# Kernel tuning notes

Measured on AMD Instinct MI355X. Metric: run time of the kernel, lower is better.

The kernel has to match this reference:

```python
import jax, jax.numpy as jnp
import numpy as np

R, S, H, B = 50000, 8, 128, 4096

def setup_inputs() -> dict:
    key = jax.random.key(0)
    ks = jax.random.split(key, 8)
    return {
        "memory": jax.random.normal(ks[0], (R, S, H), dtype=jnp.float32) * 0.02,
        "o_emb_w": jax.random.normal(ks[1], (H,), dtype=jnp.float32),
        "o_emb_r": jax.random.normal(ks[2], (B, H), dtype=jnp.float32),
        "attn_W": jax.random.normal(ks[3], (H, H), dtype=jnp.float32) * (1.0 / np.sqrt(H)),
        "sim_w": jax.random.normal(ks[4], (2 * H, 1), dtype=jnp.float32) * 0.05,
        "sim_b": jax.random.normal(ks[5], (1,), dtype=jnp.float32) * 0.05,
        "forget_w": jax.random.normal(ks[6], (2 * H, 1), dtype=jnp.float32) * 0.05,
        "o_rg": 12345,
        "d_rg": jax.random.randint(ks[7], (B,), 0, R, dtype=jnp.int32),
    }

def reference(memory, o_emb_w, o_emb_r, attn_W, sim_w, sim_b, forget_w, o_rg, d_rg):
    h = memory.shape[-1]
    # --- write (state='w'): gather one region, sigmoid forget gate, scatter update ---
    sel = memory[o_rg]                                   # [S, H]
    o_ext = jnp.broadcast_to(o_emb_w, sel.shape)         # [S, H]
    # forget_linear(cat([o_emb, mem])) with no bias
    gate = jax.nn.sigmoid(o_ext @ forget_w[:h] + sel @ forget_w[h:])  # [S, 1]
    new_slot = sel * (1.0 - gate) + o_ext * gate
    new_mem = memory.at[o_rg].set(new_slot)              # equivalent to memory*(1-pad)+o_emb*pad
    # --- read (state='r'): gather per-batch region, concat-MLP attention over slots ---
    km = new_mem[d_rg]                                   # [B, S, H]
    q = o_emb_r @ attn_W                                 # [B, H]
    kv = km @ attn_W                                     # [B, S, H] (key == value input, same projection)
    # sim_mlp = Linear(2H,1)+ReLU applied to cat([q, k]), then softmax over slot dim
    logits = jax.nn.relu((q @ sim_w[:h])[:, None, :] + kv @ sim_w[h:] + sim_b)  # [B, S, 1]
    score = jax.nn.softmax(logits, axis=-2)              # softmax over slots
    mem_out = jnp.sum(score * kv, axis=-2)               # [B, H]
    return mem_out
```

## Files before the change

### kernel.cpp

```cpp
#include <hip/hip_runtime.h>
#include <math.h>

#define H  128
#define S  8
#define BB 4

__device__ __forceinline__ float wave_sum(float v) {
    #pragma unroll
    for (int off = 32; off; off >>= 1) v += __shfl_xor(v, off, 64);
    return v;
}

__global__ __launch_bounds__(256) void fused_kernel(
        const float* __restrict__ memory,
        const float* __restrict__ o_emb_w,
        const float* __restrict__ o_emb_r,
        const float* __restrict__ attn_W,
        const float* __restrict__ sim_w,
        const float* __restrict__ sim_b,
        const float* __restrict__ forget_w,
        const int*   __restrict__ o_rg_p,
        const int*   __restrict__ d_rg,
        float* __restrict__ out) {
    __shared__ float v1s[H], v2s[H];
    __shared__ float wm_lds[BB][H];

    const int u  = threadIdx.x;
    const int wv = u >> 6;
    const int L  = u & 63;
    const int b  = blockIdx.x * BB + wv;

    const int o_rg = o_rg_p[0];
    const int r    = d_rg[b];

    const float2* src = (const float2*)(memory + (size_t)r * (S * H));
    float2 rows[S];
    #pragma unroll
    for (int s = 0; s < S; ++s) rows[s] = src[s * (H / 2) + L];
    const float2 oe = ((const float2*)o_emb_r)[(size_t)b * (H / 2) + L];

    {
        const int row = u & 127, half = u >> 7;
        const float2* wr = (const float2*)(attn_W + row * H + half * 64);
        const float2* s1 = (const float2*)(sim_w + half * 64);
        const float2* s2 = (const float2*)(sim_w + H + half * 64);
        float a1 = 0.f, a2 = 0.f;
        #pragma unroll 8
        for (int j = 0; j < 32; ++j) {
            float2 w = wr[j], x1 = s1[j], x2 = s2[j];
            a1 += w.x * x1.x + w.y * x1.y;
            a2 += w.x * x2.x + w.y * x2.y;
        }
        if (half == 0) { v1s[row] = a1; v2s[row] = a2; }
        __syncthreads();
        if (half == 1) { v1s[row] += a1; v2s[row] += a2; }
        __syncthreads();
    }

    if (r == o_rg) {
        const float2 ow = ((const float2*)o_emb_w)[L];
        const float2 f1 = ((const float2*)forget_w)[L];
        const float2 f2 = ((const float2*)(forget_w + H))[L];
        const float base = wave_sum(ow.x * f1.x + ow.y * f1.y);
        #pragma unroll
        for (int s = 0; s < S; ++s) {
            float d = wave_sum(rows[s].x * f2.x + rows[s].y * f2.y);
            float g = 1.f / (1.f + expf(-(base + d)));
            rows[s].x = rows[s].x * (1.f - g) + ow.x * g;
            rows[s].y = rows[s].y * (1.f - g) + ow.y * g;
        }
    }

    const float2 vv1 = ((const float2*)v1s)[L];
    const float2 vv2 = ((const float2*)v2s)[L];
    const float qs = wave_sum(oe.x * vv1.x + oe.y * vv1.y);
    float d2[S];
    #pragma unroll
    for (int s = 0; s < S; ++s)
        d2[s] = wave_sum(rows[s].x * vv2.x + rows[s].y * vv2.y);

    const float sb = sim_b[0];
    float l[S], m = -INFINITY;
    #pragma unroll
    for (int s = 0; s < S; ++s) { l[s] = fmaxf(qs + d2[s] + sb, 0.f); m = fmaxf(m, l[s]); }
    float p[S], psum = 0.f;
    #pragma unroll
    for (int s = 0; s < S; ++s) { p[s] = expf(l[s] - m); psum += p[s]; }
    const float inv = 1.f / psum;

    float2 wm = {0.f, 0.f};
    #pragma unroll
    for (int s = 0; s < S; ++s) {
        float ps = p[s] * inv;
        wm.x += ps * rows[s].x;
        wm.y += ps * rows[s].y;
    }
    wm_lds[wv][2 * L]     = wm.x;
    wm_lds[wv][2 * L + 1] = wm.y;
    __syncthreads();

    const float2* W2 = (const float2*)attn_W;
    const float* wmrow = wm_lds[wv];
    float2 acc = {0.f, 0.f};
    #pragma unroll 4
    for (int i = 0; i < H; ++i) {
        float2 w = W2[i * (H / 2) + L];
        float  x = wmrow[i];
        acc.x += x * w.x;
        acc.y += x * w.y;
    }
    ((float2*)out)[(size_t)b * (H / 2) + L] = acc;
}

extern "C" void kernel_launch(void* const* d_in, const int* in_sizes, int n_in,
                              void* d_out, int out_size, void* d_ws, size_t ws_size,
                              hipStream_t stream) {
    const float* memory   = (const float*)d_in[0];
    const float* o_emb_w  = (const float*)d_in[1];
    const float* o_emb_r  = (const float*)d_in[2];
    const float* attn_W   = (const float*)d_in[3];
    const float* sim_w    = (const float*)d_in[4];
    const float* sim_b    = (const float*)d_in[5];
    const float* forget_w = (const float*)d_in[6];
    const int*   o_rg     = (const int*)d_in[7];
    const int*   d_rg     = (const int*)d_in[8];
    float* out = (float*)d_out;

    const int B = in_sizes[8];

    fused_kernel<<<B / BB, 256, 0, stream>>>(
        memory, o_emb_w, o_emb_r, attn_W, sim_w, sim_b, forget_w, o_rg, d_rg, out);
}
```

Measured before the change: 271.7 us.

## Use float4 half-wave slot layout, 8 waves per block, and split-K output GEMV

Each wave now loads the gathered region as float4, so each half-wave owns four of the eight slots and per-slot reductions need only 5-step shuffles. A final exchange merges the softmax statistics and weighted sums across halves. The projection of sim_w through attn_W now uses one thread per output with float4 loads, which drops a sync. Blocks now hold 8 waves, halving the number of these precomputations across the grid, and the output GEMV splits K across the two half-waves. The cost is more shuffle exchanges, and the larger blocks may reduce scheduling flexibility.

```diff
diff --git a/kernel.cpp b/kernel.cpp
--- a/kernel.cpp
+++ b/kernel.cpp
@@ -3,7 +3,7 @@
 
 #define H  128
 #define S  8
-#define BB 4
+#define BB 8
 
 __device__ __forceinline__ float wave_sum(float v) {
     #pragma unroll
@@ -11,7 +11,7 @@
     return v;
 }
 
-__global__ __launch_bounds__(256) void fused_kernel(
+__global__ __launch_bounds__(512) void fused_kernel(
         const float* __restrict__ memory,
         const float* __restrict__ o_emb_w,
         const float* __restrict__ o_emb_r,
@@ -28,88 +28,118 @@
     const int u  = threadIdx.x;
     const int wv = u >> 6;
     const int L  = u & 63;
+    const int c  = L & 31;
+    const int hi = L >> 5;
     const int b  = blockIdx.x * BB + wv;
 
     const int o_rg = o_rg_p[0];
     const int r    = d_rg[b];
 
-    const float2* src = (const float2*)(memory + (size_t)r * (S * H));
-    float2 rows[S];
+    const float4* src4 = (const float4*)(memory + (size_t)r * (S * H));
+    float4 rows[4];
     #pragma unroll
-    for (int s = 0; s < S; ++s) rows[s] = src[s * (H / 2) + L];
+    for (int j = 0; j < 4; ++j) rows[j] = src4[j * 64 + L];
     const float2 oe = ((const float2*)o_emb_r)[(size_t)b * (H / 2) + L];
 
-    {
-        const int row = u & 127, half = u >> 7;
-        const float2* wr = (const float2*)(attn_W + row * H + half * 64);
-        const float2* s1 = (const float2*)(sim_w + half * 64);
-        const float2* s2 = (const float2*)(sim_w + H + half * 64);
-        float a1 = 0.f, a2 = 0.f;
+    if (u < 256) {
+        const int row = u & 127;
+        const float4* wr = (const float4*)(attn_W + row * H);
+        const float4* sv = (const float4*)(sim_w + (u >> 7) * H);
+        float a = 0.f;
         #pragma unroll 8
         for (int j = 0; j < 32; ++j) {
-            float2 w = wr[j], x1 = s1[j], x2 = s2[j];
-            a1 += w.x * x1.x + w.y * x1.y;
-            a2 += w.x * x2.x + w.y * x2.y;
+            float4 w = wr[j], x = sv[j];
+            a += w.x * x.x + w.y * x.y + w.z * x.z + w.w * x.w;
         }
-        if (half == 0) { v1s[row] = a1; v2s[row] = a2; }
-        __syncthreads();
-        if (half == 1) { v1s[row] += a1; v2s[row] += a2; }
-        __syncthreads();
+        if (u < 128) v1s[row] = a; else v2s[row] = a;
     }
+    __syncthreads();
 
     if (r == o_rg) {
-        const float2 ow = ((const float2*)o_emb_w)[L];
-        const float2 f1 = ((const float2*)forget_w)[L];
-        const float2 f2 = ((const float2*)(forget_w + H))[L];
-        const float base = wave_sum(ow.x * f1.x + ow.y * f1.y);
+        const float4 ow4 = ((const float4*)o_emb_w)[c];
+        const float4 f24 = ((const float4*)(forget_w + H))[c];
+        const float2 ow2 = ((const float2*)o_emb_w)[L];
+        const float2 f12 = ((const float2*)forget_w)[L];
+        const float base = wave_sum(ow2.x * f12.x + ow2.y * f12.y);
         #pragma unroll
-        for (int s = 0; s < S; ++s) {
-            float d = wave_sum(rows[s].x * f2.x + rows[s].y * f2.y);
-            float g = 1.f / (1.f + expf(-(base + d)));
-            rows[s].x = rows[s].x * (1.f - g) + ow.x * g;
-            rows[s].y = rows[s].y * (1.f - g) + ow.y * g;
+        for (int j = 0; j < 4; ++j) {
+            float v = rows[j].x * f24.x + rows[j].y * f24.y
+                    + rows[j].z * f24.z + rows[j].w * f24.w;
+            #pragma unroll
+            for (int off = 1; off <= 16; off <<= 1) v += __shfl_xor(v, off, 64);
+            float g = 1.f / (1.f + expf(-(base + v)));
+            rows[j].x = rows[j].x * (1.f - g) + ow4.x * g;
+            rows[j].y = rows[j].y * (1.f - g) + ow4.y * g;
+            rows[j].z = rows[j].z * (1.f - g) + ow4.z * g;
+            rows[j].w = rows[j].w * (1.f - g) + ow4.w * g;
         }
     }
 
     const float2 vv1 = ((const float2*)v1s)[L];
-    const float2 vv2 = ((const float2*)v2s)[L];
-    const float qs = wave_sum(oe.x * vv1.x + oe.y * vv1.y);
-    float d2[S];
+    const float  qs  = wave_sum(oe.x * vv1.x + oe.y * vv1.y);
+    const float4 vv2 = ((const float4*)v2s)[c];
+
+    float d2own[4], d2oth[4];
     #pragma unroll
-    for (int s = 0; s < S; ++s)
-        d2[s] = wave_sum(rows[s].x * vv2.x + rows[s].y * vv2.y);
+    for (int j = 0; j < 4; ++j) {
+        float v = rows[j].x * vv2.x + rows[j].y * vv2.y
+                + rows[j].z * vv2.z + rows[j].w * vv2.w;
+        #pragma unroll
+        for (int off = 1; off <= 16; off <<= 1) v += __shfl_xor(v, off, 64);
+        d2own[j] = v;
+        d2oth[j] = __shfl_xor(v, 32, 64);
+    }
 
     const float sb = sim_b[0];
-    float l[S], m = -INFINITY;
+    float lown[4], loth[4], m = -INFINITY;
     #pragma unroll
-    for (int s = 0; s < S; ++s) { l[s] = fmaxf(qs + d2[s] + sb, 0.f); m = fmaxf(m, l[s]); }
-    float p[S], psum = 0.f;
+    for (int j = 0; j < 4; ++j) {
+        lown[j] = fmaxf(qs + d2own[j] + sb, 0.f);
+        loth[j] = fmaxf(qs + d2oth[j] + sb, 0.f);
+        m = fmaxf(m, fmaxf(lown[j], loth[j]));
+    }
+    float pown[4], psum = 0.f;
     #pragma unroll
-    for (int s = 0; s < S; ++s) { p[s] = expf(l[s] - m); psum += p[s]; }
+    for (int j = 0; j < 4; ++j) {
+        pown[j] = expf(lown[j] - m);
+        psum += pown[j] + expf(loth[j] - m);
+    }
     const float inv = 1.f / psum;
 
-    float2 wm = {0.f, 0.f};
+    float4 wm = {0.f, 0.f, 0.f, 0.f};
     #pragma unroll
-    for (int s = 0; s < S; ++s) {
-        float ps = p[s] * inv;
-        wm.x += ps * rows[s].x;
-        wm.y += ps * rows[s].y;
+    for (int j = 0; j < 4; ++j) {
+        float ps = pown[j] * inv;
+        wm.x += ps * rows[j].x;
+        wm.y += ps * rows[j].y;
+        wm.z += ps * rows[j].z;
+        wm.w += ps * rows[j].w;
     }
-    wm_lds[wv][2 * L]     = wm.x;
-    wm_lds[wv][2 * L + 1] = wm.y;
+    wm.x += __shfl_xor(wm.x, 32, 64);
+    wm.y += __shfl_xor(wm.y, 32, 64);
+    wm.z += __shfl_xor(wm.z, 32, 64);
+    wm.w += __shfl_xor(wm.w, 32, 64);
+    if (hi == 0) ((float4*)wm_lds[wv])[c] = wm;
     __syncthreads();
 
-    const float2* W2 = (const float2*)attn_W;
+    const float4* W4 = (const float4*)attn_W;
     const float* wmrow = wm_lds[wv];
-    float2 acc = {0.f, 0.f};
-    #pragma unroll 4
-    for (int i = 0; i < H; ++i) {
-        float2 w = W2[i * (H / 2) + L];
+    float4 acc = {0.f, 0.f, 0.f, 0.f};
+    #pragma unroll 8
+    for (int j = 0; j < 64; ++j) {
+        int i = hi * 64 + j;
+        float4 w = W4[i * (H / 4) + c];
         float  x = wmrow[i];
         acc.x += x * w.x;
         acc.y += x * w.y;
+        acc.z += x * w.z;
+        acc.w += x * w.w;
     }
-    ((float2*)out)[(size_t)b * (H / 2) + L] = acc;
+    acc.x += __shfl_xor(acc.x, 32, 64);
+    acc.y += __shfl_xor(acc.y, 32, 64);
+    acc.z += __shfl_xor(acc.z, 32, 64);
+    acc.w += __shfl_xor(acc.w, 32, 64);
+    if (hi == 0) ((float4*)out)[(size_t)b * (H / 4) + c] = acc;
 }
 
 extern "C" void kernel_launch(void* const* d_in, const int* in_sizes, int n_in,
@@ -128,6 +158,6 @@
 
     const int B = in_sizes[8];
 
-    fused_kernel<<<B / BB, 256, 0, stream>>>(
+    fused_kernel<<<B / BB, 512, 0, stream>>>(
         memory, o_emb_w, o_emb_r, attn_W, sim_w, sim_b, forget_w, o_rg, d_rg, out);
 }
```

New measurement: 264.6 us. -2.6%, faster.
